# Kernel tuning notes

Hardware: AMD Instinct MI355X
Metric: run time of the kernel (lower is better)

The kernel has to match this reference:

```python
import jax, jax.numpy as jnp
import numpy as np

B, N, D, K = 16, 4096, 256, 2048  # batch, tokens, dim, codebook_size
COMMIT = 0.25

def setup_inputs() -> dict:
    key = jax.random.key(0)
    k1, k2 = jax.random.split(key)
    x = jax.random.normal(k1, (B, N, D), dtype=jnp.float32)
    # codebook buffer, stored as [dim, codebook_size] like lucidrains' VectorQuantize
    embed = jax.random.normal(k2, (D, K), dtype=jnp.float32)
    return {"x": x, "embed": embed}

def reference(x, embed):
    # flatten tokens: [B*N, D]
    flat = x.reshape(-1, D)
    # squared euclidean distance to every code: [B*N, K]
    dist = (jnp.sum(flat * flat, axis=1, keepdims=True)
            - 2.0 * (flat @ embed)
            + jnp.sum(embed * embed, axis=0, keepdims=True))
    idx = jnp.argmin(dist, axis=1)          # nearest code per token, [B*N]
    indices = idx.reshape(B, N)
    quantize = embed.T[indices]             # gather codes -> [B, N, D]
    # commitment loss: mse(quantize.detach(), x) * commitment
    commit_loss = jnp.mean(jnp.square(jax.lax.stop_gradient(quantize) - x)) * COMMIT
    # straight-through estimator
    quantize = x + jax.lax.stop_gradient(quantize - x)
    return quantize, commit_loss, indices
```

## Files before the change

kernel.cpp:

```cpp
#include <hip/hip_runtime.h>

#define TOK   65536
#define DIMS  256
#define NCODE 2048
#define LOSSOFF 16777216
#define IDXOFF  16777217

typedef _Float16 f16x8 __attribute__((ext_vector_type(8)));
typedef _Float16 f16x4 __attribute__((ext_vector_type(4)));
typedef float    f32x4 __attribute__((ext_vector_type(4)));

__device__ __forceinline__ void ld16(void* lds, const void* g) {
  __builtin_amdgcn_global_load_lds(
      (const __attribute__((address_space(1))) unsigned int*)g,
      (__attribute__((address_space(3))) unsigned int*)lds, 16, 0, 0);
}

__device__ __forceinline__ unsigned long long umin64(unsigned long long a,
                                                     unsigned long long b) {
  return a < b ? a : b;
}

__global__ void k_prep(const float* __restrict__ embed, float* __restrict__ embedT,
                       _Float16* __restrict__ eTh, _Float16* __restrict__ eTl) {
  __shared__ float t[32][33];
  int tx = threadIdx.x & 31, ty = threadIdx.x >> 5;
  int k0 = blockIdx.x * 32, d0 = blockIdx.y * 32;
#pragma unroll
  for (int i = 0; i < 4; ++i) {
    int d = ty + i * 8;
    t[tx][d] = embed[(size_t)(d0 + d) * NCODE + k0 + tx];
  }
  __syncthreads();
#pragma unroll
  for (int i = 0; i < 4; ++i) {
    int kl = ty + i * 8;
    float v = t[kl][tx];
    size_t o = (size_t)(k0 + kl) * DIMS + d0 + tx;
    embedT[o] = v;
    _Float16 h = (_Float16)v;
    eTh[o] = h;
    eTl[o] = (_Float16)(v - (float)h);
  }
}

__global__ void k_e2(const float* __restrict__ embed, float* __restrict__ e2) {
  int k = blockIdx.x * 256 + threadIdx.x;
  double a = 0.0;
  for (int d = 0; d < DIMS; ++d) {
    float v = embed[(size_t)d * NCODE + k];
    a += (double)v * (double)v;
  }
  e2[k] = (float)a;
}

__global__ void k_xsplit(const float* __restrict__ x, _Float16* __restrict__ xh,
                         _Float16* __restrict__ xl) {
  size_t base = (size_t)(blockIdx.x * 256 + threadIdx.x);
#pragma unroll
  for (int i = 0; i < 8; ++i) {
    size_t o = (base + (size_t)i * 524288) * 4;
    f32x4 v = *(const f32x4*)&x[o];
    f16x4 h, l;
#pragma unroll
    for (int e = 0; e < 4; ++e) {
      h[e] = (_Float16)v[e];
      l[e] = (_Float16)(v[e] - (float)h[e]);
    }
    *(f16x4*)&xh[o] = h;
    *(f16x4*)&xl[o] = l;
  }
}

__global__ void k_init(unsigned long long* __restrict__ part, float* __restrict__ out) {
  int i = blockIdx.x * 256 + threadIdx.x;
  part[i] = ~0ull;
  if (i == 0) out[LOSSOFF] = 0.0f;
}

__global__ __launch_bounds__(256, 2) void k_score(
    const _Float16* __restrict__ xh, const _Float16* __restrict__ xl,
    const _Float16* __restrict__ eTh, const _Float16* __restrict__ eTl,
    const float* __restrict__ e2, unsigned long long* __restrict__ part) {
  __shared__ _Float16 Ah[2][128 * 32];
  __shared__ _Float16 Al[2][128 * 32];
  __shared__ _Float16 Bh[2][128 * 32];
  __shared__ _Float16 Bl[2][128 * 32];

  int tid = threadIdx.x, lane = tid & 63, wid = tid >> 6;
  int wm = wid >> 1, wn = wid & 1;
  int bid = blockIdx.x;
  int wg = (bid & 7) * 1024 + (bid >> 3);
  int mblk = wg >> 4, nblk = wg & 15;
  int t0 = mblk * 128, c0 = nblk * 128;
  int col = lane & 15, kg = lane >> 4;

  float e2n[4];
#pragma unroll
  for (int n = 0; n < 4; ++n) e2n[n] = e2[c0 + wn * 64 + n * 16 + col];

  f32x4 acc[4][4] = {};

  auto stage = [&](int ck, int buf) {
    int kb = ck * 32;
#pragma unroll
    for (int q = 0; q < 2; ++q) {
      int j = wid * 2 + q;
      int row = j * 16 + (lane >> 2);
      int gl = (lane & 3) ^ ((row >> 1) & 3);
      size_t as = (size_t)(t0 + row) * DIMS + kb + gl * 8;
      size_t bs = (size_t)(c0 + row) * DIMS + kb + gl * 8;
      ld16(&Ah[buf][j * 512], &xh[as]);
      ld16(&Al[buf][j * 512], &xl[as]);
      ld16(&Bh[buf][j * 512], &eTh[bs]);
      ld16(&Bl[buf][j * 512], &eTl[bs]);
    }
  };

  stage(0, 0);
  __syncthreads();

  for (int c = 0; c < 8; ++c) {
    int buf = c & 1;
    if (c < 7) stage(c + 1, buf ^ 1);

    f16x8 ahf[4], alf[4], bhf[4], blf[4];
#pragma unroll
    for (int m = 0; m < 4; ++m) {
      int row = wm * 64 + m * 16 + col;
      int off = row * 32 + (kg ^ ((row >> 1) & 3)) * 8;
      ahf[m] = *(const f16x8*)&Ah[buf][off];
      alf[m] = *(const f16x8*)&Al[buf][off];
    }
#pragma unroll
    for (int n = 0; n < 4; ++n) {
      int row = wn * 64 + n * 16 + col;
      int off = row * 32 + (kg ^ ((row >> 1) & 3)) * 8;
      bhf[n] = *(const f16x8*)&Bh[buf][off];
      blf[n] = *(const f16x8*)&Bl[buf][off];
    }
#pragma unroll
    for (int m = 0; m < 4; ++m)
#pragma unroll
      for (int n = 0; n < 4; ++n) {
        acc[m][n] = __builtin_amdgcn_mfma_f32_16x16x32_f16(ahf[m], bhf[n], acc[m][n], 0, 0, 0);
        acc[m][n] = __builtin_amdgcn_mfma_f32_16x16x32_f16(ahf[m], blf[n], acc[m][n], 0, 0, 0);
        acc[m][n] = __builtin_amdgcn_mfma_f32_16x16x32_f16(alf[m], bhf[n], acc[m][n], 0, 0, 0);
      }
    __syncthreads();
  }

#pragma unroll
  for (int m = 0; m < 4; ++m)
#pragma unroll
    for (int r = 0; r < 4; ++r) {
      unsigned long long best = ~0ull;
#pragma unroll
      for (int n = 0; n < 4; ++n) {
        float s = e2n[n] - 2.0f * acc[m][n][r];
        unsigned u = __float_as_uint(s);
        u ^= (u & 0x80000000u) ? 0xFFFFFFFFu : 0x80000000u;
        unsigned long long key = ((unsigned long long)u << 32) |
                                 (unsigned)(c0 + wn * 64 + n * 16 + col);
        best = umin64(best, key);
      }
#pragma unroll
      for (int off = 1; off < 16; off <<= 1)
        best = umin64(best, __shfl_xor(best, off, 64));
      if (col == 0) {
        int token = t0 + wm * 64 + m * 16 + kg * 4 + r;
        atomicMin(&part[token], best);
      }
    }
}

__global__ void k_idx(const unsigned long long* __restrict__ part,
                      float* __restrict__ out, int* __restrict__ idxw) {
  int token = blockIdx.x * 256 + threadIdx.x;
  unsigned code = (unsigned)(part[token] & 0xFFFFFFFFull);
  out[IDXOFF + token] = (float)code;
  idxw[token] = (int)code;
}

__global__ void k_gather(const float* __restrict__ x, const float* __restrict__ embedT,
                         const int* __restrict__ idxw, float* __restrict__ out) {
  int wid = threadIdx.x >> 6, lane = threadIdx.x & 63;
  int gw = blockIdx.x * 4 + wid;
  float s = 0.0f;
#pragma unroll
  for (int t = 0; t < 8; ++t) {
    int token = gw * 8 + t;
    int code = idxw[token];
    f32x4 q  = *(const f32x4*)&embedT[(size_t)code * DIMS + lane * 4];
    f32x4 xv = *(const f32x4*)&x[(size_t)token * DIMS + lane * 4];
    f32x4 d = q - xv;
    *(f32x4*)&out[(size_t)token * DIMS + lane * 4] = xv + d;
    s += d[0] * d[0] + d[1] * d[1] + d[2] * d[2] + d[3] * d[3];
  }
  for (int off = 32; off; off >>= 1) s += __shfl_xor(s, off, 64);
  __shared__ float red[4];
  if (lane == 0) red[wid] = s;
  __syncthreads();
  if (threadIdx.x == 0) {
    float tsum = (red[0] + red[1] + red[2] + red[3]) * (0.25f / 16777216.0f);
    atomicAdd(&out[LOSSOFF], tsum);
  }
}

extern "C" void kernel_launch(void* const* d_in, const int* in_sizes, int n_in,
                              void* d_out, int out_size, void* d_ws, size_t ws_size,
                              hipStream_t stream) {
  const float* x     = (const float*)d_in[0];
  const float* embed = (const float*)d_in[1];
  float* out = (float*)d_out;
  _Float16* xh = (_Float16*)d_out;
  _Float16* xl = (_Float16*)((char*)d_out + (32u << 20));
  char* w = (char*)d_ws;
  _Float16* eTh    = (_Float16*)w;
  _Float16* eTl    = (_Float16*)(w + (1u << 20));
  float*    embedT = (float*)(w + (2u << 20));
  float*    e2     = (float*)(w + (4u << 20));
  unsigned long long* part = (unsigned long long*)(w + (4u << 20) + (1u << 15));
  int*      idxw   = (int*)(w + (4u << 20) + (1u << 15) + (1u << 19));

  hipLaunchKernelGGL(k_prep,   dim3(NCODE / 32, DIMS / 32), dim3(256), 0, stream, embed, embedT, eTh, eTl);
  hipLaunchKernelGGL(k_e2,     dim3(NCODE / 256),           dim3(256), 0, stream, embed, e2);
  hipLaunchKernelGGL(k_xsplit, dim3(2048),                  dim3(256), 0, stream, x, xh, xl);
  hipLaunchKernelGGL(k_init,   dim3(TOK / 256),             dim3(256), 0, stream, part, out);
  hipLaunchKernelGGL(k_score,  dim3(8192),                  dim3(256), 0, stream, xh, xl, eTh, eTl, e2, part);
  hipLaunchKernelGGL(k_idx,    dim3(TOK / 256),             dim3(256), 0, stream, part, out, idxw);
  hipLaunchKernelGGL(k_gather, dim3(2048),                  dim3(256), 0, stream, x, embedT, idxw, out);
}
```

Measured before the change: 518.0 us.

## Triple-buffer score GEMM with 256-token tiles, interleaved MFMA phases, fused small kernels

The score kernel moves to 512-thread blocks over 256x128 tiles with three LDS stages, and splits each K step into four MFMA phases separated by barriers and priority raises so loads and LDS reads overlap compute. The init kernel is folded into xsplit and the index kernel into gather, removing two launches and the idxw round trip. The larger LDS footprint (about 144KB) and one block per CU reduce occupancy, and the hand-placed waitcnts and barriers risk stalls or races if the counts are off.

Measured after the change: 554.3 us. 1.07x slower.

```diff
diff --git a/kernel.cpp b/kernel.cpp
--- a/kernel.cpp
+++ b/kernel.cpp
@@ -15,7 +15,6 @@
       (const __attribute__((address_space(1))) unsigned int*)g,
       (__attribute__((address_space(3))) unsigned int*)lds, 16, 0, 0);
 }
-
 __device__ __forceinline__ unsigned long long umin64(unsigned long long a,
                                                      unsigned long long b) {
   return a < b ? a : b;
@@ -55,8 +54,13 @@
 }
 
 __global__ void k_xsplit(const float* __restrict__ x, _Float16* __restrict__ xh,
-                         _Float16* __restrict__ xl) {
-  size_t base = (size_t)(blockIdx.x * 256 + threadIdx.x);
+                         _Float16* __restrict__ xl,
+                         unsigned long long* __restrict__ part,
+                         float* __restrict__ out) {
+  int gid = blockIdx.x * 256 + threadIdx.x;
+  if (gid < TOK) part[gid] = ~0ull;
+  if (gid == 0) out[LOSSOFF] = 0.0f;
+  size_t base = (size_t)gid;
 #pragma unroll
   for (int i = 0; i < 8; ++i) {
     size_t o = (base + (size_t)i * 524288) * 4;
@@ -72,84 +76,117 @@
   }
 }
 
-__global__ void k_init(unsigned long long* __restrict__ part, float* __restrict__ out) {
-  int i = blockIdx.x * 256 + threadIdx.x;
-  part[i] = ~0ull;
-  if (i == 0) out[LOSSOFF] = 0.0f;
-}
-
-__global__ __launch_bounds__(256, 2) void k_score(
+#define MM(ah_, al_, bh_, bl_, a_) do { \
+  a_ = __builtin_amdgcn_mfma_f32_16x16x32_f16(ah_, bh_, a_, 0, 0, 0); \
+  a_ = __builtin_amdgcn_mfma_f32_16x16x32_f16(ah_, bl_, a_, 0, 0, 0); \
+  a_ = __builtin_amdgcn_mfma_f32_16x16x32_f16(al_, bh_, a_, 0, 0, 0); } while (0)
+
+#define SBAR_PRE do { __builtin_amdgcn_sched_barrier(0); __builtin_amdgcn_s_barrier(); \
+  asm volatile("s_waitcnt lgkmcnt(0)" ::: "memory"); __builtin_amdgcn_sched_barrier(0); \
+  __builtin_amdgcn_s_setprio(1); } while (0)
+
+#define SBAR_POST do { __builtin_amdgcn_s_setprio(0); __builtin_amdgcn_sched_barrier(0); \
+  __builtin_amdgcn_s_barrier(); } while (0)
+
+__global__ __launch_bounds__(512, 1) void k_score(
     const _Float16* __restrict__ xh, const _Float16* __restrict__ xl,
     const _Float16* __restrict__ eTh, const _Float16* __restrict__ eTl,
     const float* __restrict__ e2, unsigned long long* __restrict__ part) {
-  __shared__ _Float16 Ah[2][128 * 32];
-  __shared__ _Float16 Al[2][128 * 32];
-  __shared__ _Float16 Bh[2][128 * 32];
-  __shared__ _Float16 Bl[2][128 * 32];
+  __shared__ __attribute__((aligned(16))) _Float16 Ah[3][256 * 32];
+  __shared__ __attribute__((aligned(16))) _Float16 Al[3][256 * 32];
+  __shared__ __attribute__((aligned(16))) _Float16 Bh[3][128 * 32];
+  __shared__ __attribute__((aligned(16))) _Float16 Bl[3][128 * 32];
 
   int tid = threadIdx.x, lane = tid & 63, wid = tid >> 6;
   int wm = wid >> 1, wn = wid & 1;
   int bid = blockIdx.x;
-  int wg = (bid & 7) * 1024 + (bid >> 3);
+  int wg = (bid & 7) * 512 + (bid >> 3);
   int mblk = wg >> 4, nblk = wg & 15;
-  int t0 = mblk * 128, c0 = nblk * 128;
+  int t0 = mblk * 256, c0 = nblk * 128;
   int col = lane & 15, kg = lane >> 4;
 
+  f32x4 acc[4][4] = {};
+
+  auto stageA = [&](int ck, int slot) {
+    int kb = ck * 32;
+#pragma unroll
+    for (int q = 0; q < 2; ++q) {
+      int i = q * 512 + wid * 64 + lane;
+      int row = i >> 2;
+      int g = (i & 3) ^ ((row >> 1) & 3);
+      size_t src = (size_t)(t0 + row) * DIMS + kb + g * 8;
+      ld16(&Ah[slot][(q * 512 + wid * 64) * 8], &xh[src]);
+      ld16(&Al[slot][(q * 512 + wid * 64) * 8], &xl[src]);
+    }
+  };
+  auto stageB = [&](int ck, int slot) {
+    int kb = ck * 32;
+    int i = wid * 64 + lane;
+    int row = i >> 2;
+    int g = (i & 3) ^ ((row >> 1) & 3);
+    size_t src = (size_t)(c0 + row) * DIMS + kb + g * 8;
+    ld16(&Bh[slot][(wid * 64) * 8], &eTh[src]);
+    ld16(&Bl[slot][(wid * 64) * 8], &eTl[src]);
+  };
+  auto rdA = [&](int slot, int mf, f16x8& h, f16x8& l) {
+    int row = wm * 64 + mf * 16 + col;
+    int off = row * 32 + (kg ^ ((row >> 1) & 3)) * 8;
+    h = *(const f16x8*)&Ah[slot][off];
+    l = *(const f16x8*)&Al[slot][off];
+  };
+  auto rdB = [&](int slot, int nf, f16x8& h, f16x8& l) {
+    int row = wn * 64 + nf * 16 + col;
+    int off = row * 32 + (kg ^ ((row >> 1) & 3)) * 8;
+    h = *(const f16x8*)&Bh[slot][off];
+    l = *(const f16x8*)&Bl[slot][off];
+  };
+
+  stageA(0, 0); stageB(0, 0);
+  stageA(1, 1); stageB(1, 1);
+  asm volatile("s_waitcnt vmcnt(6)" ::: "memory");
+  __builtin_amdgcn_sched_barrier(0);
+  __builtin_amdgcn_s_barrier();
+
+#pragma unroll
+  for (int c = 0; c < 8; ++c) {
+    int slot = c % 3;
+    f16x8 a0h, a0l, a1h, a1l, a2h, a2l, a3h, a3l;
+    f16x8 b0h, b0l, b1h, b1l, b2h, b2l, b3h, b3l;
+    if (c < 6) stageA(c + 2, (c + 2) % 3);
+    rdA(slot, 0, a0h, a0l); rdA(slot, 1, a1h, a1l);
+    rdB(slot, 0, b0h, b0l); rdB(slot, 1, b1h, b1l);
+    SBAR_PRE;
+    MM(a0h, a0l, b0h, b0l, acc[0][0]); MM(a0h, a0l, b1h, b1l, acc[0][1]);
+    MM(a1h, a1l, b0h, b0l, acc[1][0]); MM(a1h, a1l, b1h, b1l, acc[1][1]);
+    SBAR_POST;
+    if (c < 6) stageB(c + 2, (c + 2) % 3);
+    rdB(slot, 2, b2h, b2l); rdB(slot, 3, b3h, b3l);
+    SBAR_PRE;
+    MM(a0h, a0l, b2h, b2l, acc[0][2]); MM(a0h, a0l, b3h, b3l, acc[0][3]);
+    MM(a1h, a1l, b2h, b2l, acc[1][2]); MM(a1h, a1l, b3h, b3l, acc[1][3]);
+    SBAR_POST;
+    rdA(slot, 2, a2h, a2l); rdA(slot, 3, a3h, a3l);
+    SBAR_PRE;
+    MM(a2h, a2l, b0h, b0l, acc[2][0]); MM(a2h, a2l, b1h, b1l, acc[2][1]);
+    MM(a3h, a3l, b0h, b0l, acc[3][0]); MM(a3h, a3l, b1h, b1l, acc[3][1]);
+    SBAR_POST;
+    SBAR_PRE;
+    MM(a2h, a2l, b2h, b2l, acc[2][2]); MM(a2h, a2l, b3h, b3l, acc[2][3]);
+    MM(a3h, a3l, b2h, b2l, acc[3][2]); MM(a3h, a3l, b3h, b3l, acc[3][3]);
+    __builtin_amdgcn_s_setprio(0);
+    __builtin_amdgcn_sched_barrier(0);
+    if (c < 6) {
+      asm volatile("s_waitcnt vmcnt(6)" ::: "memory");
+    } else if (c == 6) {
+      asm volatile("s_waitcnt vmcnt(0)" ::: "memory");
+    }
+    __builtin_amdgcn_sched_barrier(0);
+    if (c < 7) __builtin_amdgcn_s_barrier();
+  }
+
   float e2n[4];
 #pragma unroll
   for (int n = 0; n < 4; ++n) e2n[n] = e2[c0 + wn * 64 + n * 16 + col];
-
-  f32x4 acc[4][4] = {};
-
-  auto stage = [&](int ck, int buf) {
-    int kb = ck * 32;
-#pragma unroll
-    for (int q = 0; q < 2; ++q) {
-      int j = wid * 2 + q;
-      int row = j * 16 + (lane >> 2);
-      int gl = (lane & 3) ^ ((row >> 1) & 3);
-      size_t as = (size_t)(t0 + row) * DIMS + kb + gl * 8;
-      size_t bs = (size_t)(c0 + row) * DIMS + kb + gl * 8;
-      ld16(&Ah[buf][j * 512], &xh[as]);
-      ld16(&Al[buf][j * 512], &xl[as]);
-      ld16(&Bh[buf][j * 512], &eTh[bs]);
-      ld16(&Bl[buf][j * 512], &eTl[bs]);
-    }
-  };
-
-  stage(0, 0);
-  __syncthreads();
-
-  for (int c = 0; c < 8; ++c) {
-    int buf = c & 1;
-    if (c < 7) stage(c + 1, buf ^ 1);
-
-    f16x8 ahf[4], alf[4], bhf[4], blf[4];
-#pragma unroll
-    for (int m = 0; m < 4; ++m) {
-      int row = wm * 64 + m * 16 + col;
-      int off = row * 32 + (kg ^ ((row >> 1) & 3)) * 8;
-      ahf[m] = *(const f16x8*)&Ah[buf][off];
-      alf[m] = *(const f16x8*)&Al[buf][off];
-    }
-#pragma unroll
-    for (int n = 0; n < 4; ++n) {
-      int row = wn * 64 + n * 16 + col;
-      int off = row * 32 + (kg ^ ((row >> 1) & 3)) * 8;
-      bhf[n] = *(const f16x8*)&Bh[buf][off];
-      blf[n] = *(const f16x8*)&Bl[buf][off];
-    }
-#pragma unroll
-    for (int m = 0; m < 4; ++m)
-#pragma unroll
-      for (int n = 0; n < 4; ++n) {
-        acc[m][n] = __builtin_amdgcn_mfma_f32_16x16x32_f16(ahf[m], bhf[n], acc[m][n], 0, 0, 0);
-        acc[m][n] = __builtin_amdgcn_mfma_f32_16x16x32_f16(ahf[m], blf[n], acc[m][n], 0, 0, 0);
-        acc[m][n] = __builtin_amdgcn_mfma_f32_16x16x32_f16(alf[m], bhf[n], acc[m][n], 0, 0, 0);
-      }
-    __syncthreads();
-  }
-
 #pragma unroll
   for (int m = 0; m < 4; ++m)
 #pragma unroll
@@ -160,37 +197,28 @@
         float s = e2n[n] - 2.0f * acc[m][n][r];
         unsigned u = __float_as_uint(s);
         u ^= (u & 0x80000000u) ? 0xFFFFFFFFu : 0x80000000u;
-        unsigned long long key = ((unsigned long long)u << 32) |
-                                 (unsigned)(c0 + wn * 64 + n * 16 + col);
-        best = umin64(best, key);
+        best = umin64(best, ((unsigned long long)u << 32) |
+                            (unsigned)(c0 + wn * 64 + n * 16 + col));
       }
 #pragma unroll
       for (int off = 1; off < 16; off <<= 1)
         best = umin64(best, __shfl_xor(best, off, 64));
-      if (col == 0) {
-        int token = t0 + wm * 64 + m * 16 + kg * 4 + r;
-        atomicMin(&part[token], best);
-      }
-    }
-}
-
-__global__ void k_idx(const unsigned long long* __restrict__ part,
-                      float* __restrict__ out, int* __restrict__ idxw) {
-  int token = blockIdx.x * 256 + threadIdx.x;
-  unsigned code = (unsigned)(part[token] & 0xFFFFFFFFull);
-  out[IDXOFF + token] = (float)code;
-  idxw[token] = (int)code;
+      if (col == 0)
+        atomicMin(&part[t0 + wm * 64 + m * 16 + kg * 4 + r], best);
+    }
 }
 
 __global__ void k_gather(const float* __restrict__ x, const float* __restrict__ embedT,
-                         const int* __restrict__ idxw, float* __restrict__ out) {
+                         const unsigned long long* __restrict__ part,
+                         float* __restrict__ out) {
   int wid = threadIdx.x >> 6, lane = threadIdx.x & 63;
   int gw = blockIdx.x * 4 + wid;
   float s = 0.0f;
 #pragma unroll
   for (int t = 0; t < 8; ++t) {
     int token = gw * 8 + t;
-    int code = idxw[token];
+    int code = (int)(part[token] & 0xFFFFFFFFull);
+    if (lane == 0) out[IDXOFF + token] = (float)code;
     f32x4 q  = *(const f32x4*)&embedT[(size_t)code * DIMS + lane * 4];
     f32x4 xv = *(const f32x4*)&x[(size_t)token * DIMS + lane * 4];
     f32x4 d = q - xv;
@@ -221,13 +249,10 @@
   float*    embedT = (float*)(w + (2u << 20));
   float*    e2     = (float*)(w + (4u << 20));
   unsigned long long* part = (unsigned long long*)(w + (4u << 20) + (1u << 15));
-  int*      idxw   = (int*)(w + (4u << 20) + (1u << 15) + (1u << 19));
 
   hipLaunchKernelGGL(k_prep,   dim3(NCODE / 32, DIMS / 32), dim3(256), 0, stream, embed, embedT, eTh, eTl);
   hipLaunchKernelGGL(k_e2,     dim3(NCODE / 256),           dim3(256), 0, stream, embed, e2);
-  hipLaunchKernelGGL(k_xsplit, dim3(2048),                  dim3(256), 0, stream, x, xh, xl);
-  hipLaunchKernelGGL(k_init,   dim3(TOK / 256),             dim3(256), 0, stream, part, out);
-  hipLaunchKernelGGL(k_score,  dim3(8192),                  dim3(256), 0, stream, xh, xl, eTh, eTl, e2, part);
-  hipLaunchKernelGGL(k_idx,    dim3(TOK / 256),             dim3(256), 0, stream, part, out, idxw);
-  hipLaunchKernelGGL(k_gather, dim3(2048),                  dim3(256), 0, stream, x, embedT, idxw, out);
-}
+  hipLaunchKernelGGL(k_xsplit, dim3(2048),                  dim3(256), 0, stream, x, xh, xl, part, out);
+  hipLaunchKernelGGL(k_score,  dim3(4096),                  dim3(512), 0, stream, xh, xl, eTh, eTl, e2, part);
+  hipLaunchKernelGGL(k_gather, dim3(2048),                  dim3(256), 0, stream, x, embedT, part, out);
+}
```
